# Kernel optimization log

Measured on AMD Instinct MI355X. Metric: run time of the kernel, lower is better.

The kernel has to match this reference:

```python
import jax, jax.numpy as jnp
import numpy as np

EMBED_DIM = 1024
NUM_HEADS = 16
HEAD_DIM = EMBED_DIM // NUM_HEADS
B, L = 32, 2049
LN_EPS = 1e-5


def setup_inputs() -> dict:
    key = jax.random.key(0)
    ks = jax.random.split(key, 11)
    s = 1.0 / np.sqrt(EMBED_DIM)
    x = jax.random.normal(ks[0], (B, L, EMBED_DIM), dtype=jnp.float32)
    Wq = jax.random.normal(ks[1], (EMBED_DIM, EMBED_DIM), dtype=jnp.float32) * s
    bq = jnp.zeros((EMBED_DIM,), dtype=jnp.float32)
    Wk = jax.random.normal(ks[2], (EMBED_DIM, EMBED_DIM), dtype=jnp.float32) * s
    bk = jnp.zeros((EMBED_DIM,), dtype=jnp.float32)
    Wv = jax.random.normal(ks[3], (EMBED_DIM, EMBED_DIM), dtype=jnp.float32) * s
    bv = jnp.zeros((EMBED_DIM,), dtype=jnp.float32)
    Wo = jax.random.normal(ks[4], (EMBED_DIM, EMBED_DIM), dtype=jnp.float32) * s
    bo = jnp.zeros((EMBED_DIM,), dtype=jnp.float32)
    ln_g = jnp.ones((EMBED_DIM,), dtype=jnp.float32)
    ln_b = jnp.zeros((EMBED_DIM,), dtype=jnp.float32)
    return {"x": x, "Wq": Wq, "bq": bq, "Wk": Wk, "bk": bk, "Wv": Wv,
            "bv": bv, "Wo": Wo, "bo": bo, "ln_g": ln_g, "ln_b": ln_b}


def reference(x, Wq, bq, Wk, bk, Wv, bv, Wo, bo, ln_g, ln_b):
    # x: [B, L, D]; CLS token attends to the other L-1 tokens (dropout = eval/identity)
    cls_tok = x[:, 0, :]              # [B, D]
    others = x[:, 1:, :]              # [B, L-1, D]
    q = cls_tok @ Wq.T + bq           # [B, D]
    k = others @ Wk.T + bk            # [B, L-1, D]
    v = others @ Wv.T + bv            # [B, L-1, D]
    q = q.reshape(q.shape[0], NUM_HEADS, HEAD_DIM)                       # [B, H, d]
    k = k.reshape(k.shape[0], k.shape[1], NUM_HEADS, HEAD_DIM)           # [B, S, H, d]
    v = v.reshape(v.shape[0], v.shape[1], NUM_HEADS, HEAD_DIM)           # [B, S, H, d]
    scores = jnp.einsum('bhd,bshd->bhs', q, k) / np.sqrt(HEAD_DIM)       # [B, H, S]
    w = jax.nn.softmax(scores, axis=-1)
    attn = jnp.einsum('bhs,bshd->bhd', w, v)                             # [B, H, d]
    attn = attn.reshape(attn.shape[0], NUM_HEADS * HEAD_DIM)             # [B, D]
    out = attn @ Wo.T + bo
    y = out + cls_tok
    mu = jnp.mean(y, axis=-1, keepdims=True)
    var = jnp.var(y, axis=-1, keepdims=True)
    return (y - mu) / jnp.sqrt(var + LN_EPS) * ln_g + ln_b               # [B, D]
```

## Files before the change

kernel.cpp:

```cpp
#include <hip/hip_runtime.h>
#include <math.h>

#define B_ 32
#define L_ 2049
#define E_ 1024
#define H_ 16
#define NT_ 8
#define STILE 256

#define OFF_Q     0
#define OFF_T     (OFF_Q + B_*E_)
#define OFF_QBK   (OFF_T + B_*H_*E_)
#define OFF_M     (OFF_QBK + B_*H_)
#define OFF_L     (OFF_M + B_*NT_*H_)
#define OFF_U     (OFF_L + B_*NT_*H_)
#define OFF_ATTN  (OFF_U + B_*H_*E_)
#define OFF_Y     (OFF_ATTN + B_*E_)
#define OFF_UP    (OFF_Y + B_*E_)

__global__ __launch_bounds__(256) void k_gemm32(const float* __restrict__ A, long long As, int mode,
                                                const float* __restrict__ W,
                                                const float* __restrict__ bias,
                                                const float* __restrict__ resid, long long Rs,
                                                float* __restrict__ C) {
    __shared__ float wls[2 * 1056];
    const int j0 = blockIdx.x * 2, tid = threadIdx.x;
    #pragma unroll
    for (int k = 0; k < 2; ++k) {
        int idx4 = k * 256 + tid;
        int row = idx4 >> 8, c4 = idx4 & 255;
        float4 v = *(const float4*)(W + (size_t)(j0 + row) * E_ + 4 * c4);
        *(float4*)&wls[row * 1056 + 4 * c4 + ((c4 >> 5) << 2)] = v;
    }
    __syncthreads();
    const int bb = tid >> 3, kseg = tid & 7;
    const long long kbase = (mode == 1) ? (long long)(j0 >> 6) * E_ : 0;
    const float* arow = A + (size_t)bb * As + kbase + kseg * 128;
    float a0 = 0.f, a1 = 0.f;
    #pragma unroll 4
    for (int i = 0; i < 32; ++i) {
        float4 av = *(const float4*)(arow + 4 * i);
        const float* wb = &wls[kseg * 132 + 4 * i];
        float4 w0 = *(const float4*)(wb);
        float4 w1 = *(const float4*)(wb + 1056);
        a0 += av.x * w0.x + av.y * w0.y + av.z * w0.z + av.w * w0.w;
        a1 += av.x * w1.x + av.y * w1.y + av.z * w1.z + av.w * w1.w;
    }
    #pragma unroll
    for (int off = 4; off; off >>= 1) {
        a0 += __shfl_down(a0, off, 8);
        a1 += __shfl_down(a1, off, 8);
    }
    if (kseg == 0) {
        float r0 = a0 + bias[j0], r1 = a1 + bias[j0 + 1];
        if (resid) {
            r0 += resid[(size_t)bb * Rs + j0];
            r1 += resid[(size_t)bb * Rs + j0 + 1];
        }
        C[(size_t)bb * E_ + j0] = r0;
        C[(size_t)bb * E_ + j0 + 1] = r1;
    }
}

__global__ __launch_bounds__(256) void k_tproj(const float* __restrict__ Wk,
                                               const float* __restrict__ bk,
                                               float* __restrict__ ws) {
    __shared__ float qs[64 * 33];
    __shared__ float wls[64 * 68];
    const int h = blockIdx.x, e0 = blockIdx.y * 64, tid = threadIdx.x;
    const float* q = ws + OFF_Q;
    #pragma unroll
    for (int k = 0; k < 8; ++k) {
        int idx = k * 256 + tid;
        int b = idx >> 6, d = idx & 63;
        qs[d * 33 + b] = q[(size_t)b * E_ + 64 * h + d];
    }
    #pragma unroll
    for (int k = 0; k < 4; ++k) {
        int idx4 = k * 256 + tid;
        int d = idx4 >> 4, c4 = idx4 & 15;
        float4 v = *(const float4*)(Wk + (size_t)(64 * h + d) * E_ + e0 + 4 * c4);
        *(float4*)&wls[d * 68 + 4 * c4] = v;
    }
    __syncthreads();
    const int el = tid & 63, bq8 = tid >> 6;
    float acc[8];
    #pragma unroll
    for (int i = 0; i < 8; ++i) acc[i] = 0.f;
    for (int d = 0; d < 64; ++d) {
        float wv = wls[d * 68 + el];
        #pragma unroll
        for (int i = 0; i < 8; ++i) acc[i] += qs[d * 33 + (bq8 * 8 + i)] * wv;
    }
    float* t = ws + OFF_T;
    #pragma unroll
    for (int i = 0; i < 8; ++i)
        t[((size_t)(bq8 * 8 + i) * H_ + h) * E_ + e0 + el] = acc[i] * 0.125f;
    if (e0 == 0 && tid < 32) {
        float s = 0.f;
        for (int d = 0; d < 64; ++d) s += qs[d * 33 + tid] * bk[64 * h + d];
        ws[OFF_QBK + tid * H_ + h] = s * 0.125f;
    }
}

__global__ __launch_bounds__(1024) void k_attn_core(const float* __restrict__ x,
                                                    float* __restrict__ ws) {
    const int tile = blockIdx.x, b = blockIdx.y, tid = threadIdx.x;
    const int s0t = tile * STILE;
    const float* tmat = ws + OFF_T + (size_t)b * H_ * E_;
    const float* xb = x + (size_t)(b * L_ + 1 + s0t) * E_;

    __shared__ float smem[16384];
    __shared__ float wl[256 * 16];
    __shared__ float pmax[64], psum[64], msh[16];

    const int lane = tid & 63, w = tid >> 6;
    const int g = lane & 3, ssub = lane >> 2;

    #pragma unroll
    for (int k = 0; k < 4; ++k) {
        int idx4 = k * 1024 + tid;
        *(float4*)&smem[4 * idx4] = *(const float4*)(tmat + 4 * idx4);
    }
    __syncthreads();

    const int eh1 = w >> 3, hh1 = (w >> 2) & 1, sq1 = w & 3;
    const int hbase1 = hh1 * 8;
    const int srow0 = sq1 * 64 + 4 * ssub;

    float acc[8][4];
    #pragma unroll
    for (int h = 0; h < 8; ++h) { acc[h][0] = 0.f; acc[h][1] = 0.f; acc[h][2] = 0.f; acc[h][3] = 0.f; }

    {
        const float* xq = xb + (size_t)srow0 * E_ + eh1 * 512 + 4 * g;
        const float* tb = &smem[hbase1 * E_ + eh1 * 512 + 4 * g];
        #pragma unroll 1
        for (int c = 0; c < 32; ++c) {
            const int e0 = 16 * c;
            float4 x0 = *(const float4*)(xq + e0);
            float4 x1 = *(const float4*)(xq + E_ + e0);
            float4 x2 = *(const float4*)(xq + 2 * E_ + e0);
            float4 x3 = *(const float4*)(xq + 3 * E_ + e0);
            #pragma unroll
            for (int h = 0; h < 8; ++h) {
                float4 t0 = *(const float4*)(tb + h * E_ + e0);
                acc[h][0] += t0.x * x0.x + t0.y * x0.y + t0.z * x0.z + t0.w * x0.w;
                acc[h][1] += t0.x * x1.x + t0.y * x1.y + t0.z * x1.z + t0.w * x1.w;
                acc[h][2] += t0.x * x2.x + t0.y * x2.y + t0.z * x2.z + t0.w * x2.w;
                acc[h][3] += t0.x * x3.x + t0.y * x3.y + t0.z * x3.z + t0.w * x3.w;
            }
        }
    }
    #pragma unroll
    for (int h = 0; h < 8; ++h) {
        #pragma unroll
        for (int k = 0; k < 4; ++k) {
            float v = acc[h][k];
            v += __shfl_xor(v, 1, 64);
            v += __shfl_xor(v, 2, 64);
            acc[h][k] = v;
        }
    }
    if (eh1 == 1) {
        #pragma unroll
        for (int k = 0; k < 4; ++k) {
            float2* dst = (float2*)&wl[(srow0 + k) * 16 + hbase1];
            if (g == 0)      dst[0] = make_float2(acc[0][k], acc[1][k]);
            else if (g == 1) dst[1] = make_float2(acc[2][k], acc[3][k]);
            else if (g == 2) dst[2] = make_float2(acc[4][k], acc[5][k]);
            else             dst[3] = make_float2(acc[6][k], acc[7][k]);
        }
    }
    __syncthreads();

    if (eh1 == 0) {
        const float* qbkp = ws + OFF_QBK + b * H_;
        #pragma unroll
        for (int k = 0; k < 4; ++k) {
            const float* src = &wl[(srow0 + k) * 16 + hbase1];
            float4 p0 = *(const float4*)(src);
            float4 p1 = *(const float4*)(src + 4);
            acc[0][k] += p0.x; acc[1][k] += p0.y; acc[2][k] += p0.z; acc[3][k] += p0.w;
            acc[4][k] += p1.x; acc[5][k] += p1.y; acc[6][k] += p1.z; acc[7][k] += p1.w;
        }
        #pragma unroll
        for (int h = 0; h < 8; ++h) {
            float qb = qbkp[hbase1 + h];
            acc[h][0] += qb; acc[h][1] += qb; acc[h][2] += qb; acc[h][3] += qb;
            float v = fmaxf(fmaxf(acc[h][0], acc[h][1]), fmaxf(acc[h][2], acc[h][3]));
            v = fmaxf(v, __shfl_xor(v, 4, 64));
            v = fmaxf(v, __shfl_xor(v, 8, 64));
            v = fmaxf(v, __shfl_xor(v, 16, 64));
            v = fmaxf(v, __shfl_xor(v, 32, 64));
            if (lane == 0) pmax[sq1 * 16 + hbase1 + h] = v;
        }
    }
    __syncthreads();
    if (tid < 16) {
        float M = pmax[tid];
        M = fmaxf(M, pmax[16 + tid]);
        M = fmaxf(M, pmax[32 + tid]);
        M = fmaxf(M, pmax[48 + tid]);
        msh[tid] = M;
        ws[OFF_M + (size_t)(b * NT_ + tile) * H_ + tid] = M;
    }
    __syncthreads();
    if (eh1 == 0) {
        #pragma unroll
        for (int h = 0; h < 8; ++h) {
            float M = msh[hbase1 + h];
            acc[h][0] = __expf(acc[h][0] - M);
            acc[h][1] = __expf(acc[h][1] - M);
            acc[h][2] = __expf(acc[h][2] - M);
            acc[h][3] = __expf(acc[h][3] - M);
        }
        #pragma unroll
        for (int k = 0; k < 4; ++k) {
            float2* dst = (float2*)&wl[(srow0 + k) * 16 + hbase1];
            if (g == 0)      dst[0] = make_float2(acc[0][k], acc[1][k]);
            else if (g == 1) dst[1] = make_float2(acc[2][k], acc[3][k]);
            else if (g == 2) dst[2] = make_float2(acc[4][k], acc[5][k]);
            else             dst[3] = make_float2(acc[6][k], acc[7][k]);
        }
        #pragma unroll
        for (int h = 0; h < 8; ++h) {
            float v = acc[h][0] + acc[h][1] + acc[h][2] + acc[h][3];
            v += __shfl_xor(v, 4, 64);
            v += __shfl_xor(v, 8, 64);
            v += __shfl_xor(v, 16, 64);
            v += __shfl_xor(v, 32, 64);
            if (lane == 0) psum[sq1 * 16 + hbase1 + h] = v;
        }
    }
    __syncthreads();
    if (tid < 16) {
        float Ls = psum[tid] + psum[16 + tid] + psum[32 + tid] + psum[48 + tid];
        ws[OFF_L + (size_t)(b * NT_ + tile) * H_ + tid] = Ls;
    }

    const int hb2 = (w >> 3) * 8;
    const int sh2 = (w >> 2) & 1;
    const int eqb = (w & 3) * 256;
    float4 acc2[8];
    #pragma unroll
    for (int j = 0; j < 8; ++j) acc2[j] = make_float4(0.f, 0.f, 0.f, 0.f);

    const int r0 = tid >> 8, c4 = tid & 255;
    float4 st0 = *(const float4*)(xb + (size_t)(r0)     * E_ + 4 * c4);
    float4 st1 = *(const float4*)(xb + (size_t)(r0 + 4) * E_ + 4 * c4);
    *(float4*)&smem[(r0)     * 1024 + 4 * c4] = st0;
    *(float4*)&smem[(r0 + 4) * 1024 + 4 * c4] = st1;
    for (int c = 0; c < 32; ++c) {
        __syncthreads();
        if (c + 1 < 32) {
            st0 = *(const float4*)(xb + (size_t)(8 * (c + 1) + r0)     * E_ + 4 * c4);
            st1 = *(const float4*)(xb + (size_t)(8 * (c + 1) + r0 + 4) * E_ + 4 * c4);
        }
        const float* A = &smem[(c & 1) * 8192];
        #pragma unroll
        for (int rr = 0; rr < 4; ++rr) {
            const int r = 4 * sh2 + rr;
            const float* wrow = &wl[(8 * c + r) * 16 + hb2];
            float4 w0 = *(const float4*)(wrow);
            float4 w1 = *(const float4*)(wrow + 4);
            float4 xv = *(const float4*)&A[r * 1024 + eqb + 4 * lane];
            acc2[0].x += w0.x * xv.x; acc2[0].y += w0.x * xv.y; acc2[0].z += w0.x * xv.z; acc2[0].w += w0.x * xv.w;
            acc2[1].x += w0.y * xv.x; acc2[1].y += w0.y * xv.y; acc2[1].z += w0.y * xv.z; acc2[1].w += w0.y * xv.w;
            acc2[2].x += w0.z * xv.x; acc2[2].y += w0.z * xv.y; acc2[2].z += w0.z * xv.z; acc2[2].w += w0.z * xv.w;
            acc2[3].x += w0.w * xv.x; acc2[3].y += w0.w * xv.y; acc2[3].z += w0.w * xv.z; acc2[3].w += w0.w * xv.w;
            acc2[4].x += w1.x * xv.x; acc2[4].y += w1.x * xv.y; acc2[4].z += w1.x * xv.z; acc2[4].w += w1.x * xv.w;
            acc2[5].x += w1.y * xv.x; acc2[5].y += w1.y * xv.y; acc2[5].z += w1.y * xv.z; acc2[5].w += w1.y * xv.w;
            acc2[6].x += w1.z * xv.x; acc2[6].y += w1.z * xv.y; acc2[6].z += w1.z * xv.z; acc2[6].w += w1.z * xv.w;
            acc2[7].x += w1.w * xv.x; acc2[7].y += w1.w * xv.y; acc2[7].z += w1.w * xv.z; acc2[7].w += w1.w * xv.w;
        }
        if (c + 1 < 32) {
            float* D = &smem[((c + 1) & 1) * 8192];
            *(float4*)&D[(r0)     * 1024 + 4 * c4] = st0;
            *(float4*)&D[(r0 + 4) * 1024 + 4 * c4] = st1;
        }
    }
    __syncthreads();
    if (sh2 == 1) {
        float* pl = &smem[((w >> 3) * 4 + (w & 3)) * 2048];
        #pragma unroll
        for (int h = 0; h < 8; ++h)
            *(float4*)&pl[h * 256 + 4 * lane] = acc2[h];
    }
    __syncthreads();
    if (sh2 == 0) {
        const float* pl = &smem[((w >> 3) * 4 + (w & 3)) * 2048];
        float* up = ws + OFF_UP + ((size_t)(b * NT_ + tile) * H_ + hb2) * E_ + eqb;
        #pragma unroll
        for (int h = 0; h < 8; ++h) {
            float4 pv = *(const float4*)&pl[h * 256 + 4 * lane];
            float4 o = make_float4(acc2[h].x + pv.x, acc2[h].y + pv.y,
                                   acc2[h].z + pv.z, acc2[h].w + pv.w);
            *(float4*)(up + (size_t)h * E_ + 4 * lane) = o;
        }
    }
}

__global__ __launch_bounds__(256) void k_combine(float* __restrict__ ws) {
    const int b = blockIdx.x, h = blockIdx.y, tid = threadIdx.x;
    float m[NT_], l[NT_], f[NT_];
    float M = -1e30f;
    #pragma unroll
    for (int tg = 0; tg < NT_; ++tg) {
        m[tg] = ws[OFF_M + (b * NT_ + tg) * H_ + h];
        l[tg] = ws[OFF_L + (b * NT_ + tg) * H_ + h];
        M = fmaxf(M, m[tg]);
    }
    float Ls = 0.f;
    #pragma unroll
    for (int tg = 0; tg < NT_; ++tg) {
        f[tg] = __expf(m[tg] - M);
        Ls += f[tg] * l[tg];
    }
    const float inv = 1.f / Ls;
    float4 a = make_float4(0.f, 0.f, 0.f, 0.f);
    #pragma unroll
    for (int tg = 0; tg < NT_; ++tg) {
        float4 v = *(const float4*)(ws + OFF_UP + (size_t)((b * NT_ + tg) * H_ + h) * E_ + 4 * tid);
        a.x += f[tg] * v.x; a.y += f[tg] * v.y; a.z += f[tg] * v.z; a.w += f[tg] * v.w;
    }
    a.x *= inv; a.y *= inv; a.z *= inv; a.w *= inv;
    *(float4*)(ws + OFF_U + (size_t)(b * H_ + h) * E_ + 4 * tid) = a;
}

__global__ __launch_bounds__(256) void k_ln(const float* __restrict__ ws,
                                            const float* __restrict__ g,
                                            const float* __restrict__ be,
                                            float* __restrict__ out) {
    const int b = blockIdx.x, tid = threadIdx.x;
    const float* y = ws + OFF_Y + (size_t)b * E_;
    float4 v = *(const float4*)(y + 4 * tid);
    float s = v.x + v.y + v.z + v.w;
    float s2 = v.x * v.x + v.y * v.y + v.z * v.z + v.w * v.w;
    for (int o = 32; o; o >>= 1) {
        s += __shfl_down(s, o, 64);
        s2 += __shfl_down(s2, o, 64);
    }
    __shared__ float rs[4], rs2[4];
    int ww = tid >> 6;
    if ((tid & 63) == 0) { rs[ww] = s; rs2[ww] = s2; }
    __syncthreads();
    float S = rs[0] + rs[1] + rs[2] + rs[3];
    float S2 = rs2[0] + rs2[1] + rs2[2] + rs2[3];
    float mean = S * (1.f / 1024.f);
    float var = S2 * (1.f / 1024.f) - mean * mean;
    float r = rsqrtf(var + 1e-5f);
    float4 gv = *(const float4*)(g + 4 * tid);
    float4 bb2 = *(const float4*)(be + 4 * tid);
    float4 o;
    o.x = (v.x - mean) * r * gv.x + bb2.x;
    o.y = (v.y - mean) * r * gv.y + bb2.y;
    o.z = (v.z - mean) * r * gv.z + bb2.z;
    o.w = (v.w - mean) * r * gv.w + bb2.w;
    *(float4*)(out + (size_t)b * E_ + 4 * tid) = o;
}

extern "C" void kernel_launch(void* const* d_in, const int* in_sizes, int n_in,
                              void* d_out, int out_size, void* d_ws, size_t ws_size,
                              hipStream_t stream) {
    const float* x  = (const float*)d_in[0];
    const float* Wq = (const float*)d_in[1];
    const float* bq = (const float*)d_in[2];
    const float* Wk = (const float*)d_in[3];
    const float* bk = (const float*)d_in[4];
    const float* Wv = (const float*)d_in[5];
    const float* bv = (const float*)d_in[6];
    const float* Wo = (const float*)d_in[7];
    const float* bo = (const float*)d_in[8];
    const float* g  = (const float*)d_in[9];
    const float* be = (const float*)d_in[10];
    float* ws = (float*)d_ws;
    float* out = (float*)d_out;

    k_gemm32<<<512, 256, 0, stream>>>(x, (long long)L_ * E_, 0, Wq, bq, nullptr, 0, ws + OFF_Q);
    k_tproj<<<dim3(16, 16), 256, 0, stream>>>(Wk, bk, ws);
    k_attn_core<<<dim3(NT_, B_), 1024, 0, stream>>>(x, ws);
    k_combine<<<dim3(B_, H_), 256, 0, stream>>>(ws);
    k_gemm32<<<512, 256, 0, stream>>>(ws + OFF_U, (long long)H_ * E_, 1, Wv, bv, nullptr, 0, ws + OFF_ATTN);
    k_gemm32<<<512, 256, 0, stream>>>(ws + OFF_ATTN, (long long)E_, 0, Wo, bo, x, (long long)L_ * E_, ws + OFF_Y);
    k_ln<<<B_, 256, 0, stream>>>(ws, g, be, out);
}
```

Baseline: 490.5 us.

## Halve attn_core block size, give each thread all 16 heads, read x directly

The attention core kernel now launches 512 threads per block instead of 1024. In the score phase each thread covers all 16 heads for 4 strided rows, so the x loads are shared across every head. The weighted-sum phase drops the double-buffered shared-memory staging of x and the cross-warp reduction. Each warp instead streams its own 128-column slice of x from global memory across all 256 rows and writes the U partials directly. This removes many barriers and LDS traffic, but raises register pressure (64 score accumulators) and relies on cache for rereads of x.

After: 490.5 us. Within noise of the previous version (-0.0%).

```diff
diff --git a/kernel.cpp b/kernel.cpp
--- a/kernel.cpp
+++ b/kernel.cpp
@@ -103,8 +103,8 @@
     }
 }
 
-__global__ __launch_bounds__(1024) void k_attn_core(const float* __restrict__ x,
-                                                    float* __restrict__ ws) {
+__global__ __launch_bounds__(512) void k_attn_core(const float* __restrict__ x,
+                                                   float* __restrict__ ws) {
     const int tile = blockIdx.x, b = blockIdx.y, tid = threadIdx.x;
     const int s0t = tile * STILE;
     const float* tmat = ws + OFF_T + (size_t)b * H_ * E_;
@@ -118,32 +118,33 @@
     const int g = lane & 3, ssub = lane >> 2;
 
     #pragma unroll
-    for (int k = 0; k < 4; ++k) {
-        int idx4 = k * 1024 + tid;
+    for (int k = 0; k < 8; ++k) {
+        int idx4 = k * 512 + tid;
         *(float4*)&smem[4 * idx4] = *(const float4*)(tmat + 4 * idx4);
     }
     __syncthreads();
 
-    const int eh1 = w >> 3, hh1 = (w >> 2) & 1, sq1 = w & 3;
-    const int hbase1 = hh1 * 8;
-    const int srow0 = sq1 * 64 + 4 * ssub;
-
-    float acc[8][4];
-    #pragma unroll
-    for (int h = 0; h < 8; ++h) { acc[h][0] = 0.f; acc[h][1] = 0.f; acc[h][2] = 0.f; acc[h][3] = 0.f; }
-
+    const int eh1 = w >> 2, sq1 = w & 3;
+    const int ehalf = eh1 * 512;
+    const int rbase1 = sq1 * 64 + ssub;
+
+    float acc[16][4];
+    #pragma unroll
+    for (int h = 0; h < 16; ++h) {
+        acc[h][0] = 0.f; acc[h][1] = 0.f; acc[h][2] = 0.f; acc[h][3] = 0.f;
+    }
     {
-        const float* xq = xb + (size_t)srow0 * E_ + eh1 * 512 + 4 * g;
-        const float* tb = &smem[hbase1 * E_ + eh1 * 512 + 4 * g];
+        const float* xq = xb + (size_t)rbase1 * E_ + ehalf + 4 * g;
+        const float* tb = &smem[ehalf + 4 * g];
         #pragma unroll 1
         for (int c = 0; c < 32; ++c) {
             const int e0 = 16 * c;
             float4 x0 = *(const float4*)(xq + e0);
-            float4 x1 = *(const float4*)(xq + E_ + e0);
-            float4 x2 = *(const float4*)(xq + 2 * E_ + e0);
-            float4 x3 = *(const float4*)(xq + 3 * E_ + e0);
+            float4 x1 = *(const float4*)(xq + 16 * E_ + e0);
+            float4 x2 = *(const float4*)(xq + 32 * E_ + e0);
+            float4 x3 = *(const float4*)(xq + 48 * E_ + e0);
             #pragma unroll
-            for (int h = 0; h < 8; ++h) {
+            for (int h = 0; h < 16; ++h) {
                 float4 t0 = *(const float4*)(tb + h * E_ + e0);
                 acc[h][0] += t0.x * x0.x + t0.y * x0.y + t0.z * x0.z + t0.w * x0.w;
                 acc[h][1] += t0.x * x1.x + t0.y * x1.y + t0.z * x1.z + t0.w * x1.w;
@@ -153,7 +154,7 @@
         }
     }
     #pragma unroll
-    for (int h = 0; h < 8; ++h) {
+    for (int h = 0; h < 16; ++h) {
         #pragma unroll
         for (int k = 0; k < 4; ++k) {
             float v = acc[h][k];
@@ -165,11 +166,11 @@
     if (eh1 == 1) {
         #pragma unroll
         for (int k = 0; k < 4; ++k) {
-            float2* dst = (float2*)&wl[(srow0 + k) * 16 + hbase1];
-            if (g == 0)      dst[0] = make_float2(acc[0][k], acc[1][k]);
-            else if (g == 1) dst[1] = make_float2(acc[2][k], acc[3][k]);
-            else if (g == 2) dst[2] = make_float2(acc[4][k], acc[5][k]);
-            else             dst[3] = make_float2(acc[6][k], acc[7][k]);
+            const int row = rbase1 + 16 * k;
+            if (g == 0)      *(float4*)&wl[row * 16 + 0]  = make_float4(acc[0][k],  acc[1][k],  acc[2][k],  acc[3][k]);
+            else if (g == 1) *(float4*)&wl[row * 16 + 4]  = make_float4(acc[4][k],  acc[5][k],  acc[6][k],  acc[7][k]);
+            else if (g == 2) *(float4*)&wl[row * 16 + 8]  = make_float4(acc[8][k],  acc[9][k],  acc[10][k], acc[11][k]);
+            else             *(float4*)&wl[row * 16 + 12] = make_float4(acc[12][k], acc[13][k], acc[14][k], acc[15][k]);
         }
     }
     __syncthreads();
@@ -177,23 +178,20 @@
     if (eh1 == 0) {
         const float* qbkp = ws + OFF_QBK + b * H_;
         #pragma unroll
-        for (int k = 0; k < 4; ++k) {
-            const float* src = &wl[(srow0 + k) * 16 + hbase1];
-            float4 p0 = *(const float4*)(src);
-            float4 p1 = *(const float4*)(src + 4);
-            acc[0][k] += p0.x; acc[1][k] += p0.y; acc[2][k] += p0.z; acc[3][k] += p0.w;
-            acc[4][k] += p1.x; acc[5][k] += p1.y; acc[6][k] += p1.z; acc[7][k] += p1.w;
-        }
-        #pragma unroll
-        for (int h = 0; h < 8; ++h) {
-            float qb = qbkp[hbase1 + h];
-            acc[h][0] += qb; acc[h][1] += qb; acc[h][2] += qb; acc[h][3] += qb;
+        for (int h = 0; h < 16; ++h) {
+            float qb = qbkp[h];
+            #pragma unroll
+            for (int k = 0; k < 4; ++k)
+                acc[h][k] += wl[(rbase1 + 16 * k) * 16 + h] + qb;
+        }
+        #pragma unroll
+        for (int h = 0; h < 16; ++h) {
             float v = fmaxf(fmaxf(acc[h][0], acc[h][1]), fmaxf(acc[h][2], acc[h][3]));
             v = fmaxf(v, __shfl_xor(v, 4, 64));
             v = fmaxf(v, __shfl_xor(v, 8, 64));
             v = fmaxf(v, __shfl_xor(v, 16, 64));
             v = fmaxf(v, __shfl_xor(v, 32, 64));
-            if (lane == 0) pmax[sq1 * 16 + hbase1 + h] = v;
+            if (lane == 0) pmax[sq1 * 16 + h] = v;
         }
     }
     __syncthreads();
@@ -208,8 +206,8 @@
     __syncthreads();
     if (eh1 == 0) {
         #pragma unroll
-        for (int h = 0; h < 8; ++h) {
-            float M = msh[hbase1 + h];
+        for (int h = 0; h < 16; ++h) {
+            float M = msh[h];
             acc[h][0] = __expf(acc[h][0] - M);
             acc[h][1] = __expf(acc[h][1] - M);
             acc[h][2] = __expf(acc[h][2] - M);
@@ -217,20 +215,20 @@
         }
         #pragma unroll
         for (int k = 0; k < 4; ++k) {
-            float2* dst = (float2*)&wl[(srow0 + k) * 16 + hbase1];
-            if (g == 0)      dst[0] = make_float2(acc[0][k], acc[1][k]);
-            else if (g == 1) dst[1] = make_float2(acc[2][k], acc[3][k]);
-            else if (g == 2) dst[2] = make_float2(acc[4][k], acc[5][k]);
-            else             dst[3] = make_float2(acc[6][k], acc[7][k]);
-        }
-        #pragma unroll
-        for (int h = 0; h < 8; ++h) {
+            const int row = rbase1 + 16 * k;
+            if (g == 0)      *(float4*)&wl[row * 16 + 0]  = make_float4(acc[0][k],  acc[1][k],  acc[2][k],  acc[3][k]);
+            else if (g == 1) *(float4*)&wl[row * 16 + 4]  = make_float4(acc[4][k],  acc[5][k],  acc[6][k],  acc[7][k]);
+            else if (g == 2) *(float4*)&wl[row * 16 + 8]  = make_float4(acc[8][k],  acc[9][k],  acc[10][k], acc[11][k]);
+            else             *(float4*)&wl[row * 16 + 12] = make_float4(acc[12][k], acc[13][k], acc[14][k], acc[15][k]);
+        }
+        #pragma unroll
+        for (int h = 0; h < 16; ++h) {
             float v = acc[h][0] + acc[h][1] + acc[h][2] + acc[h][3];
             v += __shfl_xor(v, 4, 64);
             v += __shfl_xor(v, 8, 64);
             v += __shfl_xor(v, 16, 64);
             v += __shfl_xor(v, 32, 64);
-            if (lane == 0) psum[sq1 * 16 + hbase1 + h] = v;
+            if (lane == 0) psum[sq1 * 16 + h] = v;
         }
     }
     __syncthreads();
@@ -239,65 +237,34 @@
         ws[OFF_L + (size_t)(b * NT_ + tile) * H_ + tid] = Ls;
     }
 
-    const int hb2 = (w >> 3) * 8;
-    const int sh2 = (w >> 2) & 1;
-    const int eqb = (w & 3) * 256;
-    float4 acc2[8];
-    #pragma unroll
-    for (int j = 0; j < 8; ++j) acc2[j] = make_float4(0.f, 0.f, 0.f, 0.f);
-
-    const int r0 = tid >> 8, c4 = tid & 255;
-    float4 st0 = *(const float4*)(xb + (size_t)(r0)     * E_ + 4 * c4);
-    float4 st1 = *(const float4*)(xb + (size_t)(r0 + 4) * E_ + 4 * c4);
-    *(float4*)&smem[(r0)     * 1024 + 4 * c4] = st0;
-    *(float4*)&smem[(r0 + 4) * 1024 + 4 * c4] = st1;
-    for (int c = 0; c < 32; ++c) {
-        __syncthreads();
-        if (c + 1 < 32) {
-            st0 = *(const float4*)(xb + (size_t)(8 * (c + 1) + r0)     * E_ + 4 * c4);
-            st1 = *(const float4*)(xb + (size_t)(8 * (c + 1) + r0 + 4) * E_ + 4 * c4);
-        }
-        const float* A = &smem[(c & 1) * 8192];
-        #pragma unroll
-        for (int rr = 0; rr < 4; ++rr) {
-            const int r = 4 * sh2 + rr;
-            const float* wrow = &wl[(8 * c + r) * 16 + hb2];
-            float4 w0 = *(const float4*)(wrow);
-            float4 w1 = *(const float4*)(wrow + 4);
-            float4 xv = *(const float4*)&A[r * 1024 + eqb + 4 * lane];
-            acc2[0].x += w0.x * xv.x; acc2[0].y += w0.x * xv.y; acc2[0].z += w0.x * xv.z; acc2[0].w += w0.x * xv.w;
-            acc2[1].x += w0.y * xv.x; acc2[1].y += w0.y * xv.y; acc2[1].z += w0.y * xv.z; acc2[1].w += w0.y * xv.w;
-            acc2[2].x += w0.z * xv.x; acc2[2].y += w0.z * xv.y; acc2[2].z += w0.z * xv.z; acc2[2].w += w0.z * xv.w;
-            acc2[3].x += w0.w * xv.x; acc2[3].y += w0.w * xv.y; acc2[3].z += w0.w * xv.z; acc2[3].w += w0.w * xv.w;
-            acc2[4].x += w1.x * xv.x; acc2[4].y += w1.x * xv.y; acc2[4].z += w1.x * xv.z; acc2[4].w += w1.x * xv.w;
-            acc2[5].x += w1.y * xv.x; acc2[5].y += w1.y * xv.y; acc2[5].z += w1.y * xv.z; acc2[5].w += w1.y * xv.w;
-            acc2[6].x += w1.z * xv.x; acc2[6].y += w1.z * xv.y; acc2[6].z += w1.z * xv.z; acc2[6].w += w1.z * xv.w;
-            acc2[7].x += w1.w * xv.x; acc2[7].y += w1.w * xv.y; acc2[7].z += w1.w * xv.z; acc2[7].w += w1.w * xv.w;
-        }
-        if (c + 1 < 32) {
-            float* D = &smem[((c + 1) & 1) * 8192];
-            *(float4*)&D[(r0)     * 1024 + 4 * c4] = st0;
-            *(float4*)&D[(r0 + 4) * 1024 + 4 * c4] = st1;
-        }
-    }
-    __syncthreads();
-    if (sh2 == 1) {
-        float* pl = &smem[((w >> 3) * 4 + (w & 3)) * 2048];
-        #pragma unroll
-        for (int h = 0; h < 8; ++h)
-            *(float4*)&pl[h * 256 + 4 * lane] = acc2[h];
-    }
-    __syncthreads();
-    if (sh2 == 0) {
-        const float* pl = &smem[((w >> 3) * 4 + (w & 3)) * 2048];
-        float* up = ws + OFF_UP + ((size_t)(b * NT_ + tile) * H_ + hb2) * E_ + eqb;
-        #pragma unroll
-        for (int h = 0; h < 8; ++h) {
-            float4 pv = *(const float4*)&pl[h * 256 + 4 * lane];
-            float4 o = make_float4(acc2[h].x + pv.x, acc2[h].y + pv.y,
-                                   acc2[h].z + pv.z, acc2[h].w + pv.w);
-            *(float4*)(up + (size_t)h * E_ + 4 * lane) = o;
-        }
+    const int hg = lane >> 4, cl = lane & 15;
+    float4 ua[4][2];
+    #pragma unroll
+    for (int j = 0; j < 4; ++j) {
+        ua[j][0] = make_float4(0.f, 0.f, 0.f, 0.f);
+        ua[j][1] = make_float4(0.f, 0.f, 0.f, 0.f);
+    }
+    const float* xq2 = xb + 128 * w + 8 * cl;
+    const float* wq2 = &wl[4 * hg];
+    #pragma unroll 4
+    for (int r = 0; r < 256; ++r) {
+        float4 xv0 = *(const float4*)(xq2 + (size_t)r * E_);
+        float4 xv1 = *(const float4*)(xq2 + (size_t)r * E_ + 4);
+        float4 wv = *(const float4*)(wq2 + r * 16);
+        ua[0][0].x += wv.x * xv0.x; ua[0][0].y += wv.x * xv0.y; ua[0][0].z += wv.x * xv0.z; ua[0][0].w += wv.x * xv0.w;
+        ua[0][1].x += wv.x * xv1.x; ua[0][1].y += wv.x * xv1.y; ua[0][1].z += wv.x * xv1.z; ua[0][1].w += wv.x * xv1.w;
+        ua[1][0].x += wv.y * xv0.x; ua[1][0].y += wv.y * xv0.y; ua[1][0].z += wv.y * xv0.z; ua[1][0].w += wv.y * xv0.w;
+        ua[1][1].x += wv.y * xv1.x; ua[1][1].y += wv.y * xv1.y; ua[1][1].z += wv.y * xv1.z; ua[1][1].w += wv.y * xv1.w;
+        ua[2][0].x += wv.z * xv0.x; ua[2][0].y += wv.z * xv0.y; ua[2][0].z += wv.z * xv0.z; ua[2][0].w += wv.z * xv0.w;
+        ua[2][1].x += wv.z * xv1.x; ua[2][1].y += wv.z * xv1.y; ua[2][1].z += wv.z * xv1.z; ua[2][1].w += wv.z * xv1.w;
+        ua[3][0].x += wv.w * xv0.x; ua[3][0].y += wv.w * xv0.y; ua[3][0].z += wv.w * xv0.z; ua[3][0].w += wv.w * xv0.w;
+        ua[3][1].x += wv.w * xv1.x; ua[3][1].y += wv.w * xv1.y; ua[3][1].z += wv.w * xv1.z; ua[3][1].w += wv.w * xv1.w;
+    }
+    float* up = ws + OFF_UP + ((size_t)((b * NT_ + tile) * H_ + 4 * hg)) * E_ + 128 * w + 8 * cl;
+    #pragma unroll
+    for (int j = 0; j < 4; ++j) {
+        *(float4*)(up + (size_t)j * E_)     = ua[j][0];
+        *(float4*)(up + (size_t)j * E_ + 4) = ua[j][1];
     }
 }
 
@@ -379,7 +346,7 @@
 
     k_gemm32<<<512, 256, 0, stream>>>(x, (long long)L_ * E_, 0, Wq, bq, nullptr, 0, ws + OFF_Q);
     k_tproj<<<dim3(16, 16), 256, 0, stream>>>(Wk, bk, ws);
-    k_attn_core<<<dim3(NT_, B_), 1024, 0, stream>>>(x, ws);
+    k_attn_core<<<dim3(NT_, B_), 512, 0, stream>>>(x, ws);
     k_combine<<<dim3(B_, H_), 256, 0, stream>>>(ws);
     k_gemm32<<<512, 256, 0, stream>>>(ws + OFF_U, (long long)H_ * E_, 1, Wv, bv, nullptr, 0, ws + OFF_ATTN);
     k_gemm32<<<512, 256, 0, stream>>>(ws + OFF_ATTN, (long long)E_, 0, Wo, bo, x, (long long)L_ * E_, ws + OFF_Y);
```
